# Kernel optimization log

Hardware: AMD Instinct MI355X
Metric: run time of the kernel (lower is better)

## Reference

```python
import math
import jax, jax.numpy as jnp
import numpy as np

B = 128          # batch_size (graphs)
SEQ = 128        # max_seq_len (nodes per graph)
D = 128          # input_dim
HID = 64         # enc_hidden_dim
HEADS = 4        # in_head
N = B * SEQ      # total nodes
E = 262144       # edges (avg degree 16)


def _make_pe(seq, d):
    pos = np.arange(seq, dtype=np.float32)[:, None]
    i_even = np.arange(0, d, 2, dtype=np.float32)
    pe = np.zeros((seq, d), dtype=np.float32)
    pe[:, 0::2] = np.sin(pos / 10000.0 ** (2.0 * i_even / d))
    pe[:, 1::2] = np.cos(pos / 10000.0 ** (2.0 * (i_even + 1.0) / d))
    return jnp.asarray(pe)


def setup_inputs() -> dict:
    key = jax.random.key(0)
    ks = jax.random.split(key, 10)
    s = 0.1
    return {
        "x": jax.random.normal(ks[0], (N, D), jnp.float32),
        "edge_index": jax.random.randint(ks[1], (2, E), 0, N),
        "pe": _make_pe(SEQ, D),
        "W1": jax.random.normal(ks[2], (D, HEADS * HID), jnp.float32) * s,
        "a_src1": jax.random.normal(ks[3], (HEADS, HID), jnp.float32) * s,
        "a_dst1": jax.random.normal(ks[4], (HEADS, HID), jnp.float32) * s,
        "b1": jnp.zeros((HEADS * HID,), jnp.float32),
        "W2": jax.random.normal(ks[5], (HEADS * HID, HID), jnp.float32) * s,
        "a_src2": jax.random.normal(ks[6], (1, HID), jnp.float32) * s,
        "a_dst2": jax.random.normal(ks[7], (1, HID), jnp.float32) * s,
        "b2": jnp.zeros((HID,), jnp.float32),
        "batch_size": B,
    }


def _gat_conv(x, src, dst, W, a_src, a_dst, b, heads, ch, concat, n):
    # PyG GATConv (eval mode, self-loops already appended to src/dst).
    h = (x @ W).reshape(n, heads, ch)                      # [N,H,C]
    alpha_src = jnp.einsum("nhc,hc->nh", h, a_src)         # [N,H]
    alpha_dst = jnp.einsum("nhc,hc->nh", h, a_dst)
    e = jax.nn.leaky_relu(alpha_src[src] + alpha_dst[dst], 0.2)  # [E,H]
    m = jax.ops.segment_max(e, dst, num_segments=n)        # segment softmax over dst
    ex = jnp.exp(e - m[dst])
    den = jax.ops.segment_sum(ex, dst, num_segments=n)
    alpha = ex / (den[dst] + 1e-16)                        # [E,H]
    out = jax.ops.segment_sum(h[src] * alpha[:, :, None], dst, num_segments=n)
    out = out.reshape(n, heads * ch) if concat else out.mean(axis=1)
    return out + b


def reference(x, edge_index, pe, W1, a_src1, a_dst1, b1, W2, a_src2, a_dst2, b2, batch_size):
    n = x.shape[0]
    loop = jnp.arange(n)
    src = jnp.concatenate([edge_index[0], loop])           # add self-loops (PyG default)
    dst = jnp.concatenate([edge_index[1], loop])
    # positional encoding (dropout inactive in eval)
    h = x * math.sqrt(x.shape[1]) + jnp.tile(pe, (batch_size, 1))
    h = jax.nn.elu(_gat_conv(h, src, dst, W1, a_src1, a_dst1, b1, HEADS, HID, True, n))
    out = _gat_conv(h, src, dst, W2, a_src2, a_dst2, b2, 1, HID, False, n)
    return out.reshape(batch_size, -1, out.shape[1])
```

## Files before the change

### kernel.cpp

```cpp
#include <hip/hip_runtime.h>
#include <hip/hip_bf16.h>

typedef __hip_bfloat16 bf16;

#define N_NODES 16384
#define D_IN    128
#define HID     64
#define HEADS   4
#define F1      256
#define SEQ     128
#define SLOTS   64

__device__ __forceinline__ float wave_sum(float v) {
    #pragma unroll
    for (int o = 32; o > 0; o >>= 1) v += __shfl_xor(v, o, 64);
    return v;
}
__device__ __forceinline__ float lrelu(float v) { return v > 0.f ? v : 0.2f * v; }
__device__ __forceinline__ float rdlane(float v, int l) {
    return __uint_as_float(__builtin_amdgcn_readlane(__float_as_uint(v), l));
}

#define UNPACK8(u, te, acc)                                          \
    do {                                                             \
        acc[0] += (te) * __uint_as_float((u).x << 16);               \
        acc[1] += (te) * __uint_as_float((u).x & 0xffff0000u);       \
        acc[2] += (te) * __uint_as_float((u).y << 16);               \
        acc[3] += (te) * __uint_as_float((u).y & 0xffff0000u);       \
        acc[4] += (te) * __uint_as_float((u).z << 16);               \
        acc[5] += (te) * __uint_as_float((u).z & 0xffff0000u);       \
        acc[6] += (te) * __uint_as_float((u).w << 16);               \
        acc[7] += (te) * __uint_as_float((u).w & 0xffff0000u);       \
    } while (0)

__global__ __launch_bounds__(256) void k_gemm1z(const float* __restrict__ x,
                                                const float* __restrict__ pe,
                                                const float* __restrict__ W1,
                                                const float* __restrict__ a_src1,
                                                const float* __restrict__ a_dst1,
                                                bf16* __restrict__ h,
                                                float* __restrict__ as1,
                                                float* __restrict__ ad1,
                                                int4* __restrict__ cntv) {
    int tid = threadIdx.x, lane = tid & 63, wv = tid >> 6;
    if (tid < 4) cntv[blockIdx.x * 4 + tid] = make_int4(0, 0, 0, 0);

    int base = blockIdx.x * 16;
    int j4 = lane * 4;
    float2 xr[4];
    #pragma unroll
    for (int i = 0; i < 4; i++) {
        int row = base + wv * 4 + i;
        float2 xa  = *(const float2*)(x  + (size_t)row * 128 + 2 * lane);
        float2 pea = *(const float2*)(pe + (size_t)(row & (SEQ - 1)) * 128 + 2 * lane);
        xr[i].x = xa.x * 11.313708499f + pea.x;
        xr[i].y = xa.y * 11.313708499f + pea.y;
    }
    float acc[4][4] = {};
    const float4* Wv = (const float4*)W1;
    #pragma unroll 4
    for (int k2 = 0; k2 < 64; k2++) {
        float4 w0 = Wv[(size_t)(2 * k2) * 64 + lane];
        float4 w1 = Wv[(size_t)(2 * k2 + 1) * 64 + lane];
        #pragma unroll
        for (int i = 0; i < 4; i++) {
            float a0 = rdlane(xr[i].x, k2);
            float a1 = rdlane(xr[i].y, k2);
            acc[i][0] += a0 * w0.x + a1 * w1.x;
            acc[i][1] += a0 * w0.y + a1 * w1.y;
            acc[i][2] += a0 * w0.z + a1 * w1.z;
            acc[i][3] += a0 * w0.w + a1 * w1.w;
        }
    }
    float4 asv = *(const float4*)(a_src1 + j4);
    float4 adv = *(const float4*)(a_dst1 + j4);
    #pragma unroll
    for (int i = 0; i < 4; i++) {
        int row = base + wv * 4 + i;
        union { bf16 b[4]; ushort4 u; } cv;
        cv.b[0] = __float2bfloat16(acc[i][0]);
        cv.b[1] = __float2bfloat16(acc[i][1]);
        cv.b[2] = __float2bfloat16(acc[i][2]);
        cv.b[3] = __float2bfloat16(acc[i][3]);
        *(ushort4*)(h + (size_t)row * 256 + j4) = cv.u;
        float vs = acc[i][0] * asv.x + acc[i][1] * asv.y + acc[i][2] * asv.z + acc[i][3] * asv.w;
        float vd = acc[i][0] * adv.x + acc[i][1] * adv.y + acc[i][2] * adv.z + acc[i][3] * adv.w;
        #pragma unroll
        for (int o = 1; o < 16; o <<= 1) {
            vs += __shfl_xor(vs, o);
            vd += __shfl_xor(vd, o);
        }
        if ((lane & 15) == 0) {
            as1[row * 4 + (lane >> 4)] = vs;
            ad1[row * 4 + (lane >> 4)] = vd;
        }
    }
}

__global__ __launch_bounds__(256) void k_scatter(const int* __restrict__ ei, int E, int Etot,
                                                 int* __restrict__ cnt,
                                                 int* __restrict__ esrc) {
    int e = blockIdx.x * 256 + threadIdx.x;
    if (e >= Etot) return;
    int s, d;
    if (e < E) { s = ei[e]; d = ei[E + e]; }
    else       { s = e - E; d = s; }
    int pos = atomicAdd(&cnt[d], 1);
    if (pos < SLOTS) esrc[d * SLOTS + pos] = s;
}

__global__ __launch_bounds__(256) void k_edgew1(const int* __restrict__ cnt,
                                                int* __restrict__ esrc,
                                                const float* __restrict__ as1,
                                                const float* __restrict__ ad1,
                                                float* __restrict__ et) {
    int tid = threadIdx.x, lane = tid & 63, wv = tid >> 6;
    int d = blockIdx.x * 4 + wv;
    int deg = min(cnt[d], SLOTS);
    size_t rb = (size_t)d * SLOTS + lane;
    int s = 0;
    if (lane < deg) s = esrc[rb];
    else            esrc[rb] = 0;
    float4 bv = *(const float4*)(ad1 + (size_t)d * 4);
    float t0 = 0.f, t1 = 0.f, t2 = 0.f, t3 = 0.f;
    if (lane < deg) {
        float4 av = *(const float4*)(as1 + (size_t)s * 4);
        t0 = __expf(lrelu(av.x + bv.x) - 40.f);
        t1 = __expf(lrelu(av.y + bv.y) - 40.f);
        t2 = __expf(lrelu(av.z + bv.z) - 40.f);
        t3 = __expf(lrelu(av.w + bv.w) - 40.f);
    }
    float i0 = 1.f / wave_sum(t0);
    float i1 = 1.f / wave_sum(t1);
    float i2 = 1.f / wave_sum(t2);
    float i3 = 1.f / wave_sum(t3);
    size_t eb = (size_t)d * 4 * SLOTS + lane;
    et[eb + 0 * SLOTS] = t0 * i0;
    et[eb + 1 * SLOTS] = t1 * i1;
    et[eb + 2 * SLOTS] = t2 * i2;
    et[eb + 3 * SLOTS] = t3 * i3;
}

__global__ __launch_bounds__(256) void k_edgew2(const int* __restrict__ cnt,
                                                const int* __restrict__ esrc,
                                                const float* __restrict__ as2,
                                                const float* __restrict__ ad2,
                                                float* __restrict__ et2) {
    int tid = threadIdx.x, lane = tid & 63, wv = tid >> 6;
    int d = blockIdx.x * 4 + wv;
    int deg = min(cnt[d], SLOTS);
    int s = esrc[(size_t)d * SLOTS + lane];
    float ev = as2[s];
    float adw = ad2[d];
    float t = (lane < deg) ? __expf(lrelu(ev + adw) - 40.f) : 0.f;
    float inv = 1.f / wave_sum(t);
    et2[(size_t)d * SLOTS + lane] = t * inv;
}

__global__ __launch_bounds__(256) void k_agg1_gemm2(
        const int* __restrict__ cnt, const int* __restrict__ esrc,
        const float* __restrict__ et,
        const bf16* __restrict__ h,
        const float* __restrict__ b1,
        const float* __restrict__ W2,
        const float* __restrict__ a_src2, const float* __restrict__ a_dst2,
        bf16* __restrict__ h2, float* __restrict__ as2, float* __restrict__ ad2) {
    __shared__ float hs[8][256];
    __shared__ float part[4][8][64];
    int tid = threadIdx.x, lane = tid & 63, wv = tid >> 6;
    int dbase = blockIdx.x * 8;

    int eg = lane >> 3;
    int cg_ = lane & 7;
    const bf16* hbase = h + (size_t)wv * 64 + cg_ * 8;

    int cv8 = cnt[dbase + (lane & 7)];
    float4 bb0, bb1;
    {
        const float4* b1v = (const float4*)(b1 + wv * 64 + cg_ * 8);
        bb0 = b1v[0]; bb1 = b1v[1];
    }

    const int4*   ep4 = (const int4*)(esrc + (size_t)dbase * SLOTS);
    const float4* tp4 = (const float4*)(et + ((size_t)dbase * 4 + wv) * SLOTS);

    int4   sv_n = ep4[eg];
    float4 tv_n = tp4[eg];

    #pragma unroll 2
    for (int it = 0; it < 8; it++) {
        int deg = min(__shfl(cv8, it), SLOTS);
        int4 sv = sv_n; float4 tv = tv_n;
        if (it < 7) {
            sv_n = ep4[(it + 1) * 16 + eg];
            tv_n = tp4[(it + 1) * 64 + eg];
        }

        float acc[8] = {0, 0, 0, 0, 0, 0, 0, 0};
        if (4 * eg < deg) {
            uint4 u0 = *(const uint4*)(hbase + (size_t)sv.x * 256);
            uint4 u1 = *(const uint4*)(hbase + (size_t)sv.y * 256);
            uint4 u2 = *(const uint4*)(hbase + (size_t)sv.z * 256);
            uint4 u3 = *(const uint4*)(hbase + (size_t)sv.w * 256);
            UNPACK8(u0, tv.x, acc);
            UNPACK8(u1, tv.y, acc);
            UNPACK8(u2, tv.z, acc);
            UNPACK8(u3, tv.w, acc);
        }
        for (int sub = 32; sub < deg; sub += 32) {
            int4   s2 = ep4[it * 16 + (sub >> 2) + eg];
            float4 t2 = tp4[it * 64 + (sub >> 2) + eg];
            if (sub + 4 * eg < deg) {
                uint4 u0 = *(const uint4*)(hbase + (size_t)s2.x * 256);
                uint4 u1 = *(const uint4*)(hbase + (size_t)s2.y * 256);
                uint4 u2 = *(const uint4*)(hbase + (size_t)s2.z * 256);
                uint4 u3 = *(const uint4*)(hbase + (size_t)s2.w * 256);
                UNPACK8(u0, t2.x, acc);
                UNPACK8(u1, t2.y, acc);
                UNPACK8(u2, t2.z, acc);
                UNPACK8(u3, t2.w, acc);
            }
        }
        #pragma unroll
        for (int j = 0; j < 8; j++) {
            acc[j] += __shfl_xor(acc[j], 8);
            acc[j] += __shfl_xor(acc[j], 16);
            acc[j] += __shfl_xor(acc[j], 32);
        }
        if (lane < 8) {
            int cbase = wv * 64 + lane * 8;
            float o[8];
            o[0] = acc[0] + bb0.x; o[1] = acc[1] + bb0.y;
            o[2] = acc[2] + bb0.z; o[3] = acc[3] + bb0.w;
            o[4] = acc[4] + bb1.x; o[5] = acc[5] + bb1.y;
            o[6] = acc[6] + bb1.z; o[7] = acc[7] + bb1.w;
            #pragma unroll
            for (int j = 0; j < 8; j++)
                o[j] = o[j] > 0.f ? o[j] : (__expf(o[j]) - 1.f);
            float4* dst = (float4*)&hs[it][cbase];
            dst[0] = make_float4(o[0], o[1], o[2], o[3]);
            dst[1] = make_float4(o[4], o[5], o[6], o[7]);
        }
    }
    __syncthreads();

    {
        float acc2[8] = {0, 0, 0, 0, 0, 0, 0, 0};
        const int k4base = wv * 16;
        for (int kk = 0; kk < 16; kk++) {
            int k4 = k4base + kk;
            const float* wp = W2 + (size_t)k4 * 256 + lane;
            float w0 = wp[0], w1 = wp[64], w2 = wp[128], w3 = wp[192];
            #pragma unroll
            for (int r = 0; r < 8; r++) {
                float4 u = *(const float4*)&hs[r][k4 * 4];
                acc2[r] += u.x * w0 + u.y * w1 + u.z * w2 + u.w * w3;
            }
        }
        #pragma unroll
        for (int r = 0; r < 8; r++) part[wv][r][lane] = acc2[r];
    }
    __syncthreads();
    {
        int r0 = wv * 2, r1 = r0 + 1;
        float a0 = part[0][r0][lane] + part[1][r0][lane] + part[2][r0][lane] + part[3][r0][lane];
        float a1 = part[0][r1][lane] + part[1][r1][lane] + part[2][r1][lane] + part[3][r1][lane];
        float asj = a_src2[lane], adj = a_dst2[lane];
        int n0 = dbase + r0, n1 = dbase + r1;
        h2[(size_t)n0 * 64 + lane] = __float2bfloat16(a0);
        h2[(size_t)n1 * 64 + lane] = __float2bfloat16(a1);
        float va0 = wave_sum(a0 * asj);
        float vd0 = wave_sum(a0 * adj);
        float va1 = wave_sum(a1 * asj);
        float vd1 = wave_sum(a1 * adj);
        if (lane == 0) {
            as2[n0] = va0; ad2[n0] = vd0;
            as2[n1] = va1; ad2[n1] = vd1;
        }
    }
}

__global__ __launch_bounds__(256) void k_agg2(const int* __restrict__ cnt,
                                              const int* __restrict__ esrc,
                                              const float* __restrict__ et2,
                                              const bf16* __restrict__ h2,
                                              const float* __restrict__ b2v,
                                              float* __restrict__ out) {
    int tid = threadIdx.x, lane = tid & 63, wv = tid >> 6;
    int d = blockIdx.x * 4 + wv;
    int eg = lane >> 3, cg_ = lane & 7;
    const bf16* hbase = h2 + cg_ * 8;
    const int4*   ep4 = (const int4*)(esrc + (size_t)d * SLOTS);
    const float4* tp4 = (const float4*)(et2 + (size_t)d * SLOTS);

    int4   sv = ep4[eg];
    float4 tv = tp4[eg];
    int deg = min(cnt[d], SLOTS);

    float acc[8] = {0, 0, 0, 0, 0, 0, 0, 0};
    if (4 * eg < deg) {
        uint4 u0 = *(const uint4*)(hbase + (size_t)sv.x * 64);
        uint4 u1 = *(const uint4*)(hbase + (size_t)sv.y * 64);
        uint4 u2 = *(const uint4*)(hbase + (size_t)sv.z * 64);
        uint4 u3 = *(const uint4*)(hbase + (size_t)sv.w * 64);
        UNPACK8(u0, tv.x, acc);
        UNPACK8(u1, tv.y, acc);
        UNPACK8(u2, tv.z, acc);
        UNPACK8(u3, tv.w, acc);
    }
    for (int sub = 32; sub < deg; sub += 32) {
        int4   s2 = ep4[(sub >> 2) + eg];
        float4 t2 = tp4[(sub >> 2) + eg];
        if (sub + 4 * eg < deg) {
            uint4 u0 = *(const uint4*)(hbase + (size_t)s2.x * 64);
            uint4 u1 = *(const uint4*)(hbase + (size_t)s2.y * 64);
            uint4 u2 = *(const uint4*)(hbase + (size_t)s2.z * 64);
            uint4 u3 = *(const uint4*)(hbase + (size_t)s2.w * 64);
            UNPACK8(u0, t2.x, acc);
            UNPACK8(u1, t2.y, acc);
            UNPACK8(u2, t2.z, acc);
            UNPACK8(u3, t2.w, acc);
        }
    }
    #pragma unroll
    for (int j = 0; j < 8; j++) {
        acc[j] += __shfl_xor(acc[j], 8);
        acc[j] += __shfl_xor(acc[j], 16);
        acc[j] += __shfl_xor(acc[j], 32);
    }
    if (lane < 8) {
        int cbase = lane * 8;
        float o[8];
        #pragma unroll
        for (int j = 0; j < 8; j++) o[j] = acc[j] + b2v[cbase + j];
        float4* dst = (float4*)(out + (size_t)d * 64 + cbase);
        dst[0] = make_float4(o[0], o[1], o[2], o[3]);
        dst[1] = make_float4(o[4], o[5], o[6], o[7]);
    }
}

extern "C" void kernel_launch(void* const* d_in, const int* in_sizes, int n_in,
                              void* d_out, int out_size, void* d_ws, size_t ws_size,
                              hipStream_t stream) {
    const float* x    = (const float*)d_in[0];
    const int*   ei   = (const int*)  d_in[1];
    const float* pe   = (const float*)d_in[2];
    const float* W1   = (const float*)d_in[3];
    const float* a_s1 = (const float*)d_in[4];
    const float* a_d1 = (const float*)d_in[5];
    const float* b1   = (const float*)d_in[6];
    const float* W2   = (const float*)d_in[7];
    const float* a_s2 = (const float*)d_in[8];
    const float* a_d2 = (const float*)d_in[9];
    const float* b2   = (const float*)d_in[10];

    const int E    = in_sizes[1] / 2;
    const int n    = N_NODES;
    const int Etot = E + n;

    char* p = (char*)d_ws;
    auto alloc = [&](size_t bytes) -> void* {
        void* r = (void*)p;
        p += (bytes + 255) & ~(size_t)255;
        return r;
    };
    int*   cnt     = (int*)  alloc((size_t)n * 4);
    int*   esrc    = (int*)  alloc((size_t)n * SLOTS * 4);
    float* et      = (float*)alloc((size_t)n * HEADS * SLOTS * 4);
    bf16*  h       = (bf16*) alloc((size_t)n * F1 * 2);
    float* as1     = (float*)alloc((size_t)n * HEADS * 4);
    float* ad1     = (float*)alloc((size_t)n * HEADS * 4);
    bf16*  h2      = (bf16*) alloc((size_t)n * HID * 2);
    float* as2     = (float*)alloc((size_t)n * 4);
    float* ad2     = (float*)alloc((size_t)n * 4);
    float* et2     = et;

    int eblocks = (Etot + 255) / 256;

    k_gemm1z    <<<n / 16, 256, 0, stream>>>(x, pe, W1, a_s1, a_d1, h, as1, ad1, (int4*)cnt);
    k_scatter   <<<eblocks, 256, 0, stream>>>(ei, E, Etot, cnt, esrc);
    k_edgew1    <<<n / 4, 256, 0, stream>>>(cnt, esrc, as1, ad1, et);
    k_agg1_gemm2<<<n / 8, 256, 0, stream>>>(cnt, esrc, et, h, b1,
                                            W2, a_s2, a_d2, h2, as2, ad2);
    k_edgew2    <<<n / 4, 256, 0, stream>>>(cnt, esrc, as2, ad2, et2);
    k_agg2      <<<n / 4, 256, 0, stream>>>(cnt, esrc, et2, h2, b2, (float*)d_out);
}
```

Before: 174.8 us.

## Fuse edge softmax weight kernels into aggregation kernels via shared memory

Removes the separate edge-weight kernels for both GAT layers and computes the per-destination softmax weights inside the aggregation kernels, staging them in shared memory instead of a global edge-weight buffer. This drops two launches and the global write and read of the edge-weight array. Uninitialized slots are no longer zeroed, so source indices are masked with N_NODES-1 to keep gathers in bounds. The shared scratch is reused for the GEMM partial sums, and the weight computation now sits serially before the gather phase.

```diff
diff --git a/kernel.cpp b/kernel.cpp
--- a/kernel.cpp
+++ b/kernel.cpp
@@ -109,67 +109,18 @@
     if (pos < SLOTS) esrc[d * SLOTS + pos] = s;
 }
 
-__global__ __launch_bounds__(256) void k_edgew1(const int* __restrict__ cnt,
-                                                int* __restrict__ esrc,
-                                                const float* __restrict__ as1,
-                                                const float* __restrict__ ad1,
-                                                float* __restrict__ et) {
-    int tid = threadIdx.x, lane = tid & 63, wv = tid >> 6;
-    int d = blockIdx.x * 4 + wv;
-    int deg = min(cnt[d], SLOTS);
-    size_t rb = (size_t)d * SLOTS + lane;
-    int s = 0;
-    if (lane < deg) s = esrc[rb];
-    else            esrc[rb] = 0;
-    float4 bv = *(const float4*)(ad1 + (size_t)d * 4);
-    float t0 = 0.f, t1 = 0.f, t2 = 0.f, t3 = 0.f;
-    if (lane < deg) {
-        float4 av = *(const float4*)(as1 + (size_t)s * 4);
-        t0 = __expf(lrelu(av.x + bv.x) - 40.f);
-        t1 = __expf(lrelu(av.y + bv.y) - 40.f);
-        t2 = __expf(lrelu(av.z + bv.z) - 40.f);
-        t3 = __expf(lrelu(av.w + bv.w) - 40.f);
-    }
-    float i0 = 1.f / wave_sum(t0);
-    float i1 = 1.f / wave_sum(t1);
-    float i2 = 1.f / wave_sum(t2);
-    float i3 = 1.f / wave_sum(t3);
-    size_t eb = (size_t)d * 4 * SLOTS + lane;
-    et[eb + 0 * SLOTS] = t0 * i0;
-    et[eb + 1 * SLOTS] = t1 * i1;
-    et[eb + 2 * SLOTS] = t2 * i2;
-    et[eb + 3 * SLOTS] = t3 * i3;
-}
-
-__global__ __launch_bounds__(256) void k_edgew2(const int* __restrict__ cnt,
-                                                const int* __restrict__ esrc,
-                                                const float* __restrict__ as2,
-                                                const float* __restrict__ ad2,
-                                                float* __restrict__ et2) {
-    int tid = threadIdx.x, lane = tid & 63, wv = tid >> 6;
-    int d = blockIdx.x * 4 + wv;
-    int deg = min(cnt[d], SLOTS);
-    int s = esrc[(size_t)d * SLOTS + lane];
-    float ev = as2[s];
-    float adw = ad2[d];
-    float t = (lane < deg) ? __expf(lrelu(ev + adw) - 40.f) : 0.f;
-    float inv = 1.f / wave_sum(t);
-    et2[(size_t)d * SLOTS + lane] = t * inv;
-}
-
 __global__ __launch_bounds__(256) void k_agg1_gemm2(
         const int* __restrict__ cnt, const int* __restrict__ esrc,
-        const float* __restrict__ et,
+        const float* __restrict__ as1, const float* __restrict__ ad1,
         const bf16* __restrict__ h,
         const float* __restrict__ b1,
         const float* __restrict__ W2,
         const float* __restrict__ a_src2, const float* __restrict__ a_dst2,
         bf16* __restrict__ h2, float* __restrict__ as2, float* __restrict__ ad2) {
     __shared__ float hs[8][256];
-    __shared__ float part[4][8][64];
+    __shared__ float scr[2048];
     int tid = threadIdx.x, lane = tid & 63, wv = tid >> 6;
     int dbase = blockIdx.x * 8;
-
     int eg = lane >> 3;
     int cg_ = lane & 7;
     const bf16* hbase = h + (size_t)wv * 64 + cg_ * 8;
@@ -181,20 +132,28 @@
         bb0 = b1v[0]; bb1 = b1v[1];
     }
 
-    const int4*   ep4 = (const int4*)(esrc + (size_t)dbase * SLOTS);
-    const float4* tp4 = (const float4*)(et + ((size_t)dbase * 4 + wv) * SLOTS);
-
-    int4   sv_n = ep4[eg];
-    float4 tv_n = tp4[eg];
-
+    #pragma unroll 4
+    for (int it = 0; it < 8; it++) {
+        int d = dbase + it;
+        int deg = min(__shfl(cv8, it), SLOTS);
+        int s = esrc[(size_t)d * SLOTS + lane] & (N_NODES - 1);
+        float av = as1[(size_t)s * 4 + wv];
+        float adw = ad1[d * 4 + wv];
+        float t = (lane < deg) ? __expf(lrelu(av + adw) - 40.f) : 0.f;
+        float inv = 1.f / wave_sum(t);
+        scr[(it * 4 + wv) * 64 + lane] = t * inv;
+    }
+
+    const int4* ep4 = (const int4*)(esrc + (size_t)dbase * SLOTS);
+    int4 sv_n = ep4[eg];
     #pragma unroll 2
     for (int it = 0; it < 8; it++) {
         int deg = min(__shfl(cv8, it), SLOTS);
-        int4 sv = sv_n; float4 tv = tv_n;
-        if (it < 7) {
-            sv_n = ep4[(it + 1) * 16 + eg];
-            tv_n = tp4[(it + 1) * 64 + eg];
-        }
+        int4 sv = sv_n;
+        if (it < 7) sv_n = ep4[(it + 1) * 16 + eg];
+        sv.x &= N_NODES - 1; sv.y &= N_NODES - 1;
+        sv.z &= N_NODES - 1; sv.w &= N_NODES - 1;
+        const float* tsr = &scr[(it * 4 + wv) * 64];
 
         float acc[8] = {0, 0, 0, 0, 0, 0, 0, 0};
         if (4 * eg < deg) {
@@ -202,19 +161,22 @@
             uint4 u1 = *(const uint4*)(hbase + (size_t)sv.y * 256);
             uint4 u2 = *(const uint4*)(hbase + (size_t)sv.z * 256);
             uint4 u3 = *(const uint4*)(hbase + (size_t)sv.w * 256);
+            float4 tv = *(const float4*)(tsr + 4 * eg);
             UNPACK8(u0, tv.x, acc);
             UNPACK8(u1, tv.y, acc);
             UNPACK8(u2, tv.z, acc);
             UNPACK8(u3, tv.w, acc);
         }
         for (int sub = 32; sub < deg; sub += 32) {
-            int4   s2 = ep4[it * 16 + (sub >> 2) + eg];
-            float4 t2 = tp4[it * 64 + (sub >> 2) + eg];
+            int4 s2 = ep4[it * 16 + (sub >> 2) + eg];
+            s2.x &= N_NODES - 1; s2.y &= N_NODES - 1;
+            s2.z &= N_NODES - 1; s2.w &= N_NODES - 1;
             if (sub + 4 * eg < deg) {
                 uint4 u0 = *(const uint4*)(hbase + (size_t)s2.x * 256);
                 uint4 u1 = *(const uint4*)(hbase + (size_t)s2.y * 256);
                 uint4 u2 = *(const uint4*)(hbase + (size_t)s2.z * 256);
                 uint4 u3 = *(const uint4*)(hbase + (size_t)s2.w * 256);
+                float4 t2 = *(const float4*)(tsr + sub + 4 * eg);
                 UNPACK8(u0, t2.x, acc);
                 UNPACK8(u1, t2.y, acc);
                 UNPACK8(u2, t2.z, acc);
@@ -258,13 +220,15 @@
             }
         }
         #pragma unroll
-        for (int r = 0; r < 8; r++) part[wv][r][lane] = acc2[r];
+        for (int r = 0; r < 8; r++) scr[(wv * 8 + r) * 64 + lane] = acc2[r];
     }
     __syncthreads();
     {
         int r0 = wv * 2, r1 = r0 + 1;
-        float a0 = part[0][r0][lane] + part[1][r0][lane] + part[2][r0][lane] + part[3][r0][lane];
-        float a1 = part[0][r1][lane] + part[1][r1][lane] + part[2][r1][lane] + part[3][r1][lane];
+        float a0 = scr[(0 * 8 + r0) * 64 + lane] + scr[(1 * 8 + r0) * 64 + lane]
+                 + scr[(2 * 8 + r0) * 64 + lane] + scr[(3 * 8 + r0) * 64 + lane];
+        float a1 = scr[(0 * 8 + r1) * 64 + lane] + scr[(1 * 8 + r1) * 64 + lane]
+                 + scr[(2 * 8 + r1) * 64 + lane] + scr[(3 * 8 + r1) * 64 + lane];
         float asj = a_src2[lane], adj = a_dst2[lane];
         int n0 = dbase + r0, n1 = dbase + r1;
         h2[(size_t)n0 * 64 + lane] = __float2bfloat16(a0);
@@ -282,20 +246,29 @@
 
 __global__ __launch_bounds__(256) void k_agg2(const int* __restrict__ cnt,
                                               const int* __restrict__ esrc,
-                                              const float* __restrict__ et2,
+                                              const float* __restrict__ as2,
+                                              const float* __restrict__ ad2,
                                               const bf16* __restrict__ h2,
                                               const float* __restrict__ b2v,
                                               float* __restrict__ out) {
+    __shared__ float ts[4][64];
     int tid = threadIdx.x, lane = tid & 63, wv = tid >> 6;
     int d = blockIdx.x * 4 + wv;
+    int deg = min(cnt[d], SLOTS);
     int eg = lane >> 3, cg_ = lane & 7;
     const bf16* hbase = h2 + cg_ * 8;
-    const int4*   ep4 = (const int4*)(esrc + (size_t)d * SLOTS);
-    const float4* tp4 = (const float4*)(et2 + (size_t)d * SLOTS);
-
-    int4   sv = ep4[eg];
-    float4 tv = tp4[eg];
-    int deg = min(cnt[d], SLOTS);
+    const int4* ep4 = (const int4*)(esrc + (size_t)d * SLOTS);
+
+    int4 sv = ep4[eg];
+    sv.x &= N_NODES - 1; sv.y &= N_NODES - 1;
+    sv.z &= N_NODES - 1; sv.w &= N_NODES - 1;
+
+    int s = esrc[(size_t)d * SLOTS + lane] & (N_NODES - 1);
+    float av = as2[s];
+    float adw = ad2[d];
+    float t = (lane < deg) ? __expf(lrelu(av + adw) - 40.f) : 0.f;
+    float inv = 1.f / wave_sum(t);
+    ts[wv][lane] = t * inv;
 
     float acc[8] = {0, 0, 0, 0, 0, 0, 0, 0};
     if (4 * eg < deg) {
@@ -303,19 +276,22 @@
         uint4 u1 = *(const uint4*)(hbase + (size_t)sv.y * 64);
         uint4 u2 = *(const uint4*)(hbase + (size_t)sv.z * 64);
         uint4 u3 = *(const uint4*)(hbase + (size_t)sv.w * 64);
+        float4 tv = *(const float4*)&ts[wv][4 * eg];
         UNPACK8(u0, tv.x, acc);
         UNPACK8(u1, tv.y, acc);
         UNPACK8(u2, tv.z, acc);
         UNPACK8(u3, tv.w, acc);
     }
     for (int sub = 32; sub < deg; sub += 32) {
-        int4   s2 = ep4[(sub >> 2) + eg];
-        float4 t2 = tp4[(sub >> 2) + eg];
+        int4 s2 = ep4[(sub >> 2) + eg];
+        s2.x &= N_NODES - 1; s2.y &= N_NODES - 1;
+        s2.z &= N_NODES - 1; s2.w &= N_NODES - 1;
         if (sub + 4 * eg < deg) {
             uint4 u0 = *(const uint4*)(hbase + (size_t)s2.x * 64);
             uint4 u1 = *(const uint4*)(hbase + (size_t)s2.y * 64);
             uint4 u2 = *(const uint4*)(hbase + (size_t)s2.z * 64);
             uint4 u3 = *(const uint4*)(hbase + (size_t)s2.w * 64);
+            float4 t2 = *(const float4*)&ts[wv][sub + 4 * eg];
             UNPACK8(u0, t2.x, acc);
             UNPACK8(u1, t2.y, acc);
             UNPACK8(u2, t2.z, acc);
@@ -366,22 +342,18 @@
     };
     int*   cnt     = (int*)  alloc((size_t)n * 4);
     int*   esrc    = (int*)  alloc((size_t)n * SLOTS * 4);
-    float* et      = (float*)alloc((size_t)n * HEADS * SLOTS * 4);
     bf16*  h       = (bf16*) alloc((size_t)n * F1 * 2);
     float* as1     = (float*)alloc((size_t)n * HEADS * 4);
     float* ad1     = (float*)alloc((size_t)n * HEADS * 4);
     bf16*  h2      = (bf16*) alloc((size_t)n * HID * 2);
     float* as2     = (float*)alloc((size_t)n * 4);
     float* ad2     = (float*)alloc((size_t)n * 4);
-    float* et2     = et;
 
     int eblocks = (Etot + 255) / 256;
 
     k_gemm1z    <<<n / 16, 256, 0, stream>>>(x, pe, W1, a_s1, a_d1, h, as1, ad1, (int4*)cnt);
     k_scatter   <<<eblocks, 256, 0, stream>>>(ei, E, Etot, cnt, esrc);
-    k_edgew1    <<<n / 4, 256, 0, stream>>>(cnt, esrc, as1, ad1, et);
-    k_agg1_gemm2<<<n / 8, 256, 0, stream>>>(cnt, esrc, et, h, b1,
+    k_agg1_gemm2<<<n / 8, 256, 0, stream>>>(cnt, esrc, as1, ad1, h, b1,
                                             W2, a_s2, a_d2, h2, as2, ad2);
-    k_edgew2    <<<n / 4, 256, 0, stream>>>(cnt, esrc, as2, ad2, et2);
-    k_agg2      <<<n / 4, 256, 0, stream>>>(cnt, esrc, et2, h2, b2, (float*)d_out);
-}
+    k_agg2      <<<n / 4, 256, 0, stream>>>(cnt, esrc, as2, ad2, h2, b2, (float*)d_out);
+}
```

Measured after the change: 170.7 us. 1.02x faster.
